# Optimization experiments

Hardware: AMD Instinct MI355X
Metric: run time of the kernel (lower is better)

The kernel has to match this reference:

```python
import jax, jax.numpy as jnp
import numpy as np

NEG_INF = jnp.float32(-jnp.inf)


def setup_inputs() -> dict:
    key = jax.random.key(0)
    ks = jax.random.split(key, 5)
    B, S, E, A = 4, 2048, 1024, 1024
    x = jax.random.normal(ks[0], (B, S, E), dtype=jnp.float32)
    # nn.Linear weights are [out, in]; scale ~ kaiming-uniform-ish
    sc = 1.0 / np.sqrt(E)
    Wq = jax.random.normal(ks[1], (A, E), dtype=jnp.float32) * sc
    Wk = jax.random.normal(ks[2], (A, E), dtype=jnp.float32) * sc
    Wv = jax.random.normal(ks[3], (A, E), dtype=jnp.float32) * sc
    Wo = jax.random.normal(ks[4], (A, A), dtype=jnp.float32) * sc
    padding_mask = jnp.ones((B, S), dtype=bool)  # 1 = valid token
    return {"x": x, "Wq": Wq, "Wk": Wk, "Wv": Wv, "Wo": Wo,
            "padding_mask": padding_mask}


def reference(x, Wq, Wk, Wv, Wo, padding_mask):
    # Single-head causal self-attention (is_bidirectional=False, dropout=0.0)
    B, S, E = x.shape
    q = jnp.einsum('bse,ae->bsa', x, Wq)
    k = jnp.einsum('bse,ae->bsa', x, Wk)
    v = jnp.einsum('bse,ae->bsa', x, Wv)
    d = q.shape[-1]
    scores = jnp.einsum('bqa,bka->bqk', q, k) / jnp.sqrt(jnp.float32(d))
    causal = jnp.triu(jnp.ones((S, S), dtype=bool), k=1)          # [S,S]
    pad = jnp.logical_not(padding_mask)[:, None, :]               # [B,1,S]
    mask = causal[None, :, :] | pad                               # [B,S,S]
    scores = jnp.where(mask, NEG_INF, scores)
    attn = jax.nn.softmax(scores, axis=-1)
    out = jnp.einsum('bqk,bka->bqa', attn, v)
    return jnp.einsum('bqa,oa->bqo', out, Wo)
```

## Files before the change

### kernel.cpp

```cpp
#include <hip/hip_runtime.h>
#include <hip/hip_bf16.h>


typedef __bf16 bf16x8 __attribute__((ext_vector_type(8)));
typedef float f32x4 __attribute__((ext_vector_type(4)));
typedef unsigned short us8 __attribute__((ext_vector_type(8)));

__device__ __forceinline__ unsigned short f2bf(float f) {
    unsigned u = __builtin_bit_cast(unsigned, f);
    u += 0x7fffu + ((u >> 16) & 1u);
    return (unsigned short)(u >> 16);
}

__device__ __forceinline__ void gload16(const void* g, void* l) {
    __builtin_amdgcn_global_load_lds((const __attribute__((address_space(1))) void*)g,
                                     (__attribute__((address_space(3))) void*)l,
                                     16, 0, 0);
}

__global__ void conv_bf16(const float* __restrict__ in, unsigned short* __restrict__ out, int n8) {
    int i = blockIdx.x * blockDim.x + threadIdx.x;
    if (i >= n8) return;
    long long b = (long long)i * 8;
    float4 a = *(const float4*)(in + b);
    float4 c = *(const float4*)(in + b + 4);
    us8 r = { f2bf(a.x), f2bf(a.y), f2bf(a.z), f2bf(a.w),
              f2bf(c.x), f2bf(c.y), f2bf(c.z), f2bf(c.w) };
    *(us8*)(out + b) = r;
}

#define BM 128
#define BN 128
#define BK 64

__global__ __launch_bounds__(256, 2) void gemm_bt(
    const unsigned short* __restrict__ A, const unsigned short* __restrict__ B,
    void* __restrict__ C,
    int lda, int ldb, int ldc, int Ktiles,
    long long sAz, long long sBz, long long sCz,
    int ep, float scale, int tri_skip, int causal_kv)
{
    const int mt = blockIdx.x, nt = blockIdx.y, z = blockIdx.z;
    if (tri_skip && nt > mt) return;
    int ktiles = Ktiles;
    if (causal_kv) { int lim = (mt + 1) * (BM / BK); if (lim < ktiles) ktiles = lim; }

    A += (long long)z * sAz;
    B += (long long)z * sBz;

    __shared__ __align__(16) unsigned short smem[BM * BK + BN * BK];

    const int tid  = threadIdx.x;
    const int lane = tid & 63;
    const int wave = tid >> 6;
    const int wm = wave >> 1, wn = wave & 1;

    const int srow   = lane >> 3;
    const int schunk = (lane & 7) ^ (srow & 7);

    f32x4 acc[4][4];
#pragma unroll
    for (int i = 0; i < 4; ++i)
#pragma unroll
        for (int j = 0; j < 4; ++j) acc[i][j] = f32x4{0.f, 0.f, 0.f, 0.f};

    const long long m0 = (long long)mt * BM;
    const long long n0 = (long long)nt * BN;

    for (int kt = 0; kt < ktiles; ++kt) {
        const long long kb = (long long)kt * BK + schunk * 8;
#pragma unroll
        for (int j = 0; j < 4; ++j) {
            const int seg = wave * 4 + j;
            gload16(A + (m0 + seg * 8 + srow) * lda + kb, &smem[seg * 512]);
        }
#pragma unroll
        for (int j = 0; j < 4; ++j) {
            const int seg = wave * 4 + j;
            gload16(B + (n0 + seg * 8 + srow) * ldb + kb, &smem[8192 + seg * 512]);
        }
        __syncthreads();
#pragma unroll
        for (int kk = 0; kk < 2; ++kk) {
            bf16x8 av[4], bv[4];
            const int cb = kk * 4 + (lane >> 4);
#pragma unroll
            for (int mi = 0; mi < 4; ++mi) {
                const int r = wm * 64 + mi * 16 + (lane & 15);
                av[mi] = *(const bf16x8*)&smem[r * 64 + ((cb ^ (r & 7)) * 8)];
            }
#pragma unroll
            for (int ni = 0; ni < 4; ++ni) {
                const int r = wn * 64 + ni * 16 + (lane & 15);
                bv[ni] = *(const bf16x8*)&smem[8192 + r * 64 + ((cb ^ (r & 7)) * 8)];
            }
#pragma unroll
            for (int mi = 0; mi < 4; ++mi)
#pragma unroll
                for (int ni = 0; ni < 4; ++ni)
                    acc[mi][ni] = __builtin_amdgcn_mfma_f32_16x16x32_bf16(
                        av[mi], bv[ni], acc[mi][ni], 0, 0, 0);
        }
        __syncthreads();
    }

    const int rl = (lane >> 4) * 4;
    const int cl = lane & 15;
    if (ep == 1) {
        float* Cp = (float*)C + (long long)z * sCz;
#pragma unroll
        for (int mi = 0; mi < 4; ++mi)
#pragma unroll
            for (int ni = 0; ni < 4; ++ni) {
                const long long m = m0 + wm * 64 + mi * 16 + rl;
                const long long n = n0 + wn * 64 + ni * 16 + cl;
#pragma unroll
                for (int j = 0; j < 4; ++j)
                    Cp[(m + j) * ldc + n] = acc[mi][ni][j] * scale;
            }
    } else if (ep == 3 && z == 2) {
        unsigned short* Cp = (unsigned short*)C + 2 * sCz;
#pragma unroll
        for (int mi = 0; mi < 4; ++mi)
#pragma unroll
            for (int ni = 0; ni < 4; ++ni) {
                const long long m = m0 + wm * 64 + mi * 16 + rl;
                const long long n = n0 + wn * 64 + ni * 16 + cl;
#pragma unroll
                for (int j = 0; j < 4; ++j) {
                    const long long mm = m + j;
                    Cp[((mm >> 11) << 21) + n * 2048 + (mm & 2047)] = f2bf(acc[mi][ni][j]);
                }
            }
    } else {
        unsigned short* Cp = (unsigned short*)C + (long long)z * sCz;
#pragma unroll
        for (int mi = 0; mi < 4; ++mi)
#pragma unroll
            for (int ni = 0; ni < 4; ++ni) {
                const long long m = m0 + wm * 64 + mi * 16 + rl;
                const long long n = n0 + wn * 64 + ni * 16 + cl;
#pragma unroll
                for (int j = 0; j < 4; ++j)
                    Cp[(m + j) * ldc + n] = f2bf(acc[mi][ni][j]);
            }
    }
}

__global__ __launch_bounds__(256) void softmax_causal(const float* __restrict__ S,
                                                      unsigned short* __restrict__ P)
{
    const int r = blockIdx.x;
    const int q = r & 2047;
    const float* row = S + (long long)r * 2048;
    unsigned short* prow = P + (long long)r * 4096;
    const int t = threadIdx.x;
    const int base = t * 8;
    const int lane = t & 63, wave = t >> 6;

    float4 v0 = *(const float4*)(row + base);
    float4 v1 = *(const float4*)(row + base + 4);
    float v[8] = {v0.x, v0.y, v0.z, v0.w, v1.x, v1.y, v1.z, v1.w};

    float mx = -3.0e38f;
#pragma unroll
    for (int j = 0; j < 8; ++j) if (base + j <= q) mx = fmaxf(mx, v[j]);
#pragma unroll
    for (int off = 32; off; off >>= 1) mx = fmaxf(mx, __shfl_xor(mx, off));

    __shared__ float red[8];
    if (lane == 0) red[wave] = mx;
    __syncthreads();
    mx = fmaxf(fmaxf(red[0], red[1]), fmaxf(red[2], red[3]));

    float e[8];
    float s = 0.f;
#pragma unroll
    for (int j = 0; j < 8; ++j) {
        e[j] = (base + j <= q) ? __expf(v[j] - mx) : 0.f;
        s += e[j];
    }
#pragma unroll
    for (int off = 32; off; off >>= 1) s += __shfl_xor(s, off);
    if (lane == 0) red[4 + wave] = s;
    __syncthreads();
    const float inv = 1.f / (red[4] + red[5] + red[6] + red[7]);

    us8 o;
#pragma unroll
    for (int j = 0; j < 8; ++j) o[j] = f2bf(e[j] * inv);
    *(us8*)(prow + base) = o;
}

extern "C" void kernel_launch(void* const* d_in, const int* in_sizes, int n_in,
                              void* d_out, int out_size, void* d_ws, size_t ws_size,
                              hipStream_t stream)
{
    const float* x  = (const float*)d_in[0];
    const float* Wq = (const float*)d_in[1];
    const float* Wk = (const float*)d_in[2];
    const float* Wv = (const float*)d_in[3];
    const float* Wo = (const float*)d_in[4];

    unsigned short* xb = (unsigned short*)d_ws;
    unsigned short* wb = xb + (8ll << 20);
    unsigned short* Qb = wb + (4ll << 20);
    unsigned short* Kb = Qb + (8ll << 20);
    unsigned short* Vt = Kb + (8ll << 20);
    float* Sc = (float*)(Vt + (8ll << 20));
    unsigned short* P = (unsigned short*)Sc;

    conv_bf16<<<4096, 256, 0, stream>>>(x, xb, 1048576);
    conv_bf16<<<512, 256, 0, stream>>>(Wq, wb, 131072);
    conv_bf16<<<512, 256, 0, stream>>>(Wk, wb + (1 << 20), 131072);
    conv_bf16<<<512, 256, 0, stream>>>(Wv, wb + (2 << 20), 131072);
    conv_bf16<<<512, 256, 0, stream>>>(Wo, wb + (3 << 20), 131072);

    gemm_bt<<<dim3(64, 8, 3), 256, 0, stream>>>(xb, wb, Qb,
        1024, 1024, 1024, 16, 0ll, 1ll << 20, 8ll << 20, 3, 1.f, 0, 0);

    gemm_bt<<<dim3(16, 16, 4), 256, 0, stream>>>(Qb, Kb, Sc,
        1024, 1024, 2048, 16, 1ll << 21, 1ll << 21, 1ll << 22, 1, 0.03125f, 1, 0);

    softmax_causal<<<8192, 256, 0, stream>>>(Sc, P);

    gemm_bt<<<dim3(16, 8, 4), 256, 0, stream>>>(P, Vt, Qb,
        4096, 2048, 1024, 32, 8ll << 20, 1ll << 21, 1ll << 21, 0, 1.f, 0, 1);

    gemm_bt<<<dim3(64, 8, 1), 256, 0, stream>>>(Qb, wb + (3 << 20), d_out,
        1024, 1024, 1024, 16, 0ll, 0ll, 0ll, 1, 1.f, 0, 0);
}
```

Before: 268.6 us.

## Store scores as bf16, softmax in place over causal region, merge QKV launches

The score GEMM now writes pre-scaled bf16 scores instead of fp32. The softmax runs in place and only touches the causal 128-column blocks that the PV GEMM later reads, which cuts score-buffer traffic substantially. The Q/K/V projections become one launch over a concatenated weight matrix with per-tile output routing, the four weight conversions become one launch, and gemm_bt's launch bound is raised to 4 blocks per CU. Rounding raw scores to bf16 before softmax loses some precision, and the tighter register budget may cause spills.

```diff
diff --git a/kernel.cpp b/kernel.cpp
--- a/kernel.cpp
+++ b/kernel.cpp
@@ -11,6 +11,10 @@
     u += 0x7fffu + ((u >> 16) & 1u);
     return (unsigned short)(u >> 16);
 }
+__device__ __forceinline__ float bf2f(unsigned short h) {
+    unsigned u = (unsigned)h << 16;
+    return __builtin_bit_cast(float, u);
+}
 
 __device__ __forceinline__ void gload16(const void* g, void* l) {
     __builtin_amdgcn_global_load_lds((const __attribute__((address_space(1))) void*)g,
@@ -18,9 +22,8 @@
                                      16, 0, 0);
 }
 
-__global__ void conv_bf16(const float* __restrict__ in, unsigned short* __restrict__ out, int n8) {
+__global__ void conv_x(const float* __restrict__ in, unsigned short* __restrict__ out) {
     int i = blockIdx.x * blockDim.x + threadIdx.x;
-    if (i >= n8) return;
     long long b = (long long)i * 8;
     float4 a = *(const float4*)(in + b);
     float4 c = *(const float4*)(in + b + 4);
@@ -29,11 +32,25 @@
     *(us8*)(out + b) = r;
 }
 
+__global__ void conv_w(const float* __restrict__ w0, const float* __restrict__ w1,
+                       const float* __restrict__ w2, const float* __restrict__ w3,
+                       unsigned short* __restrict__ out) {
+    const int z = blockIdx.z;
+    const float* in = (z == 0) ? w0 : (z == 1) ? w1 : (z == 2) ? w2 : w3;
+    int i = blockIdx.x * blockDim.x + threadIdx.x;
+    long long b = (long long)i * 8;
+    float4 a = *(const float4*)(in + b);
+    float4 c = *(const float4*)(in + b + 4);
+    us8 r = { f2bf(a.x), f2bf(a.y), f2bf(a.z), f2bf(a.w),
+              f2bf(c.x), f2bf(c.y), f2bf(c.z), f2bf(c.w) };
+    *(us8*)(out + (long long)z * (1 << 20) + b) = r;
+}
+
 #define BM 128
 #define BN 128
 #define BK 64
 
-__global__ __launch_bounds__(256, 2) void gemm_bt(
+__global__ __launch_bounds__(256, 4) void gemm_bt(
     const unsigned short* __restrict__ A, const unsigned short* __restrict__ B,
     void* __restrict__ C,
     int lda, int ldb, int ldc, int Ktiles,
@@ -118,8 +135,8 @@
                 for (int j = 0; j < 4; ++j)
                     Cp[(m + j) * ldc + n] = acc[mi][ni][j] * scale;
             }
-    } else if (ep == 3 && z == 2) {
-        unsigned short* Cp = (unsigned short*)C + 2 * sCz;
+    } else if (ep == 3) {
+        unsigned short* Cp = (unsigned short*)C;
 #pragma unroll
         for (int mi = 0; mi < 4; ++mi)
 #pragma unroll
@@ -129,7 +146,11 @@
 #pragma unroll
                 for (int j = 0; j < 4; ++j) {
                     const long long mm = m + j;
-                    Cp[((mm >> 11) << 21) + n * 2048 + (mm & 2047)] = f2bf(acc[mi][ni][j]);
+                    const unsigned short val = f2bf(acc[mi][ni][j]);
+                    if (nt < 8)        Cp[mm * 1024 + n] = val;
+                    else if (nt < 16)  Cp[(8ll << 20) + mm * 1024 + (n - 1024)] = val;
+                    else               Cp[(16ll << 20) + ((mm >> 11) << 21)
+                                          + (n - 2048) * 2048 + (mm & 2047)] = val;
                 }
             }
     } else {
@@ -142,29 +163,34 @@
                 const long long n = n0 + wn * 64 + ni * 16 + cl;
 #pragma unroll
                 for (int j = 0; j < 4; ++j)
-                    Cp[(m + j) * ldc + n] = f2bf(acc[mi][ni][j]);
-            }
-    }
-}
-
-__global__ __launch_bounds__(256) void softmax_causal(const float* __restrict__ S,
-                                                      unsigned short* __restrict__ P)
+                    Cp[(m + j) * ldc + n] = f2bf(acc[mi][ni][j] * scale);
+            }
+    }
+}
+
+__global__ __launch_bounds__(256) void softmax_causal(unsigned short* __restrict__ S)
 {
     const int r = blockIdx.x;
     const int q = r & 2047;
-    const float* row = S + (long long)r * 2048;
-    unsigned short* prow = P + (long long)r * 4096;
+    const int bound = ((q >> 7) + 1) * 128;
+    unsigned short* row = S + (long long)r * 2048;
     const int t = threadIdx.x;
     const int base = t * 8;
     const int lane = t & 63, wave = t >> 6;
-
-    float4 v0 = *(const float4*)(row + base);
-    float4 v1 = *(const float4*)(row + base + 4);
-    float v[8] = {v0.x, v0.y, v0.z, v0.w, v1.x, v1.y, v1.z, v1.w};
+    const bool act = base < bound;
+
+    float v[8];
+    if (act) {
+        us8 u = *(const us8*)(row + base);
+#pragma unroll
+        for (int j = 0; j < 8; ++j) v[j] = bf2f(u[j]);
+    }
 
     float mx = -3.0e38f;
-#pragma unroll
-    for (int j = 0; j < 8; ++j) if (base + j <= q) mx = fmaxf(mx, v[j]);
+    if (act) {
+#pragma unroll
+        for (int j = 0; j < 8; ++j) if (base + j <= q) mx = fmaxf(mx, v[j]);
+    }
 #pragma unroll
     for (int off = 32; off; off >>= 1) mx = fmaxf(mx, __shfl_xor(mx, off));
 
@@ -177,7 +203,7 @@
     float s = 0.f;
 #pragma unroll
     for (int j = 0; j < 8; ++j) {
-        e[j] = (base + j <= q) ? __expf(v[j] - mx) : 0.f;
+        e[j] = (act && base + j <= q) ? __expf(v[j] - mx) : 0.f;
         s += e[j];
     }
 #pragma unroll
@@ -186,10 +212,12 @@
     __syncthreads();
     const float inv = 1.f / (red[4] + red[5] + red[6] + red[7]);
 
-    us8 o;
-#pragma unroll
-    for (int j = 0; j < 8; ++j) o[j] = f2bf(e[j] * inv);
-    *(us8*)(prow + base) = o;
+    if (act) {
+        us8 o;
+#pragma unroll
+        for (int j = 0; j < 8; ++j) o[j] = f2bf(e[j] * inv);
+        *(us8*)(row + base) = o;
+    }
 }
 
 extern "C" void kernel_launch(void* const* d_in, const int* in_sizes, int n_in,
@@ -207,25 +235,21 @@
     unsigned short* Qb = wb + (4ll << 20);
     unsigned short* Kb = Qb + (8ll << 20);
     unsigned short* Vt = Kb + (8ll << 20);
-    float* Sc = (float*)(Vt + (8ll << 20));
-    unsigned short* P = (unsigned short*)Sc;
-
-    conv_bf16<<<4096, 256, 0, stream>>>(x, xb, 1048576);
-    conv_bf16<<<512, 256, 0, stream>>>(Wq, wb, 131072);
-    conv_bf16<<<512, 256, 0, stream>>>(Wk, wb + (1 << 20), 131072);
-    conv_bf16<<<512, 256, 0, stream>>>(Wv, wb + (2 << 20), 131072);
-    conv_bf16<<<512, 256, 0, stream>>>(Wo, wb + (3 << 20), 131072);
-
-    gemm_bt<<<dim3(64, 8, 3), 256, 0, stream>>>(xb, wb, Qb,
-        1024, 1024, 1024, 16, 0ll, 1ll << 20, 8ll << 20, 3, 1.f, 0, 0);
-
-    gemm_bt<<<dim3(16, 16, 4), 256, 0, stream>>>(Qb, Kb, Sc,
-        1024, 1024, 2048, 16, 1ll << 21, 1ll << 21, 1ll << 22, 1, 0.03125f, 1, 0);
-
-    softmax_causal<<<8192, 256, 0, stream>>>(Sc, P);
-
-    gemm_bt<<<dim3(16, 8, 4), 256, 0, stream>>>(P, Vt, Qb,
-        4096, 2048, 1024, 32, 8ll << 20, 1ll << 21, 1ll << 21, 0, 1.f, 0, 1);
+    unsigned short* Sb = Vt + (8ll << 20);
+
+    conv_x<<<4096, 256, 0, stream>>>(x, xb);
+    conv_w<<<dim3(512, 1, 4), 256, 0, stream>>>(Wq, Wk, Wv, Wo, wb);
+
+    gemm_bt<<<dim3(64, 24, 1), 256, 0, stream>>>(xb, wb, Qb,
+        1024, 1024, 1024, 16, 0ll, 0ll, 0ll, 3, 1.f, 0, 0);
+
+    gemm_bt<<<dim3(16, 16, 4), 256, 0, stream>>>(Qb, Kb, Sb,
+        1024, 1024, 2048, 16, 1ll << 21, 1ll << 21, 1ll << 22, 0, 0.03125f, 1, 0);
+
+    softmax_causal<<<8192, 256, 0, stream>>>(Sb);
+
+    gemm_bt<<<dim3(16, 8, 4), 256, 0, stream>>>(Sb, Vt, Qb,
+        2048, 2048, 1024, 32, 1ll << 22, 1ll << 21, 1ll << 21, 0, 1.f, 0, 1);
 
     gemm_bt<<<dim3(64, 8, 1), 256, 0, stream>>>(Qb, wb + (3 << 20), d_out,
         1024, 1024, 1024, 16, 0ll, 0ll, 0ll, 1, 1.f, 0, 0);
```

Result: slower. 275.2 us (+2.4%).
